# Performance work log

Measured on AMD Instinct MI355X. Metric: run time of the kernel, lower is better.

## Reference

```python
import jax, jax.numpy as jnp
import numpy as np
import math

B, NI, NU, D, H, MAXNB, T = 1024, 50000, 20000, 256, 4, 20, 1000


def _cosine_sqrt_ab():
    t = jnp.linspace(0.0, T, T + 1) / T
    ab = jnp.cos((t + 0.008) / 1.008 * math.pi / 2) ** 2
    ab = ab / ab[0]
    ab = ab[1:]
    return jnp.sqrt(ab), jnp.sqrt(1.0 - ab)


def _ln(x, g, b, eps=1e-5):
    m = jnp.mean(x, -1, keepdims=True)
    v = jnp.var(x, -1, keepdims=True)
    return (x - m) / jnp.sqrt(v + eps) * g + b


def _mha(q, k, v, wqkv, bqkv, wo, bo):
    # torch nn.MultiheadAttention (batch_first) with packed in_proj
    d = q.shape[-1]
    dh = d // H
    wq, wk, wv = jnp.split(wqkv, 3, axis=0)
    bq, bk, bv = jnp.split(bqkv, 3, axis=0)
    def heads(x, w, bb):
        y = x @ w.T + bb
        return y.reshape(x.shape[0], x.shape[1], H, dh).transpose(0, 2, 1, 3)
    qh, kh, vh = heads(q, wq, bq), heads(k, wk, bk), heads(v, wv, bv)
    att = jax.nn.softmax(jnp.einsum('bhqd,bhkd->bhqk', qh, kh) / math.sqrt(dh), axis=-1)
    o = jnp.einsum('bhqk,bhkd->bhqd', att, vh)
    o = o.transpose(0, 2, 1, 3).reshape(q.shape[0], q.shape[1], d)
    return o @ wo.T + bo


def setup_inputs() -> dict:
    key = jax.random.key(0)
    ks = iter(jax.random.split(key, 64))
    p = lambda shape, s=0.02: jax.random.normal(next(ks), shape, jnp.float32) * s
    inp = {}
    inp['x0'] = (jax.random.uniform(next(ks), (B, NI)) < 0.05).astype(jnp.float32)
    inp['user_ids'] = jax.random.randint(next(ks), (B,), 0, NU)
    inp['t'] = jax.random.randint(next(ks), (B,), 0, T)
    inp['noise'] = jax.random.normal(next(ks), (B, D), jnp.float32)
    inp['neighbor_idx'] = jax.random.randint(next(ks), (NU, MAXNB), 0, NI)
    inp['item_emb'] = p((NI, D), 0.01)
    inp['enc_w1'] = p((2 * D, NI), 0.01); inp['enc_b1'] = jnp.zeros((2 * D,))
    inp['enc_w2'] = p((D, 2 * D)); inp['enc_b2'] = jnp.zeros((D,))
    inp['dec_w1'] = p((2 * D, D)); inp['dec_b1'] = jnp.zeros((2 * D,))
    inp['dec_w2'] = p((NI, 2 * D)); inp['dec_b2'] = jnp.zeros((NI,))
    inp['up_w'] = p((D, D)); inp['up_b'] = jnp.zeros((D,))
    inp['ip_w'] = p((D, D)); inp['ip_b'] = jnp.zeros((D,))
    inp['te_w1'] = p((32, 1)); inp['te_b1'] = jnp.zeros((32,))
    inp['te_w2'] = p((D, 32)); inp['te_b2'] = jnp.zeros((D,))
    inp['ca_wqkv'] = p((3 * D, D)); inp['ca_bqkv'] = jnp.zeros((3 * D,))
    inp['ca_wo'] = p((D, D)); inp['ca_bo'] = jnp.zeros((D,))
    inp['sa_wqkv'] = p((3 * D, D)); inp['sa_bqkv'] = jnp.zeros((3 * D,))
    inp['sa_wo'] = p((D, D)); inp['sa_bo'] = jnp.zeros((D,))
    inp['n1_g'] = jnp.ones((D,)); inp['n1_b'] = jnp.zeros((D,))
    inp['n2_g'] = jnp.ones((D,)); inp['n2_b'] = jnp.zeros((D,))
    inp['ff_w1'] = p((2 * D, D)); inp['ff_b1'] = jnp.zeros((2 * D,))
    inp['ff_w2'] = p((D, 2 * D)); inp['ff_b2'] = jnp.zeros((D,))
    return inp


def reference(x0, user_ids, t, noise, neighbor_idx, item_emb,
              enc_w1, enc_b1, enc_w2, enc_b2, dec_w1, dec_b1, dec_w2, dec_b2,
              up_w, up_b, ip_w, ip_b, te_w1, te_b1, te_w2, te_b2,
              ca_wqkv, ca_bqkv, ca_wo, ca_bo, sa_wqkv, sa_bqkv, sa_wo, sa_bo,
              n1_g, n1_b, n2_g, n2_b, ff_w1, ff_b1, ff_w2, ff_b2):
    gelu = lambda x: jax.nn.gelu(x, approximate=False)
    # encoder: (B, NI) -> (B, D)
    z0 = gelu(x0 @ enc_w1.T + enc_b1) @ enc_w2.T + enc_b2
    sqrt_ab, sqrt_1ab = _cosine_sqrt_ab()
    z_t = sqrt_ab[t][:, None] * z0 + sqrt_1ab[t][:, None] * noise
    # vectorized padded neighbor gather: (B, MAXNB, D)
    nb = item_emb[neighbor_idx[user_ids]]
    t_norm = t.astype(jnp.float32) / T
    # denoiser
    q = (z_t @ up_w.T + up_b)[:, None, :]
    kv = nb @ ip_w.T + ip_b
    te = jax.nn.silu(t_norm[:, None] @ te_w1.T + te_b1) @ te_w2.T + te_b2
    q = q + te[:, None, :]
    ca = _mha(q, kv, kv, ca_wqkv, ca_bqkv, ca_wo, ca_bo)
    h = _ln(q + ca, n1_g, n1_b)[:, 0, :]
    sa = _mha(h[:, None], h[:, None], h[:, None], sa_wqkv, sa_bqkv, sa_wo, sa_bo)[:, 0, :]
    h = _ln(h + sa, n2_g, n2_b)
    z_pred = h + (gelu(h @ ff_w1.T + ff_b1) @ ff_w2.T + ff_b2)
    diff_loss = jnp.mean((z_pred - z0) ** 2)
    logits = gelu(z0 @ dec_w1.T + dec_b1) @ dec_w2.T + dec_b2
    recon = jnp.mean(jax.nn.softplus(logits) - logits * x0)
    return diff_loss + 0.1 * recon
```

## Files before the change

### kernel.cpp

```cpp
#include <hip/hip_runtime.h>
#include <math.h>

#define NI   50000
#define Tt   1000
#define KP   50176
#define MW   1568

typedef __bf16 bf16x8 __attribute__((ext_vector_type(8)));
typedef float  f32x4  __attribute__((ext_vector_type(4)));

__device__ __forceinline__ unsigned short f2bf(float f) {
  unsigned u = __float_as_uint(f);
  u += 0x7FFFu + ((u >> 16) & 1u);
  return (unsigned short)(u >> 16);
}
__device__ __forceinline__ float bf2f(unsigned short u) {
  return __uint_as_float(((unsigned)u) << 16);
}
__device__ __forceinline__ unsigned pack2(float a, float b) {
  return (unsigned)f2bf(a) | ((unsigned)f2bf(b) << 16);
}
__device__ __forceinline__ f32x4 mfma16(const unsigned short* a, const unsigned short* b, f32x4 c) {
  typedef unsigned short u16x8 __attribute__((ext_vector_type(8)));
  u16x8 av = *(const u16x8*)a;
  u16x8 bv = *(const u16x8*)b;
  return __builtin_amdgcn_mfma_f32_16x16x32_bf16(
      __builtin_bit_cast(bf16x8, av), __builtin_bit_cast(bf16x8, bv), c, 0, 0, 0);
}
__device__ __forceinline__ float gelu_f(float x) {
  return 0.5f * x * (1.f + erff(x * 0.70710678118654752f));
}

#define GLD16(gsrc, ldst) __builtin_amdgcn_global_load_lds( \
    (const __attribute__((address_space(1))) unsigned int*)(const void*)(gsrc), \
    (__attribute__((address_space(3))) unsigned int*)(void*)(ldst), 16, 0, 0)
#define GLD4(gsrc, ldst) __builtin_amdgcn_global_load_lds( \
    (const __attribute__((address_space(1))) unsigned int*)(const void*)(gsrc), \
    (__attribute__((address_space(3))) unsigned int*)(void*)(ldst), 4, 0, 0)

#define PIPE_FENCE() __builtin_amdgcn_sched_barrier(0)
#define RAW_BAR()    __builtin_amdgcn_s_barrier()

#define PC_BM 6272
#define PC_W1 19072

__global__ __launch_bounds__(256) void prep_crit(
    const float* __restrict__ x0, unsigned int* __restrict__ xmask,
    unsigned int* __restrict__ xmaskT,
    const float* __restrict__ enc_w1, unsigned short* __restrict__ w1b)
{
  __shared__ unsigned int T[32][8];
  const int id = blockIdx.x, tid = threadIdx.x;
  if (id < PC_BM) {
    const int rg = id / 196, wc = id % 196;
    const int r0 = rg * 32, w0 = wc * 8;
    const int rr = tid >> 3, wd = tid & 7;
    const int row = r0 + rr;
    const int gw = w0 + wd;
    const int cb = gw * 32;
    const float* rp = x0 + (size_t)row * NI + cb;
    unsigned wv = 0;
    if (cb + 32 <= NI) {
#pragma unroll
      for (int k = 0; k < 8; ++k) {
        float4 v = *(const float4*)(rp + k * 4);
        wv |= (v.x != 0.f ? 1u : 0u) << (k * 4) |
              (v.y != 0.f ? 2u : 0u) << (k * 4) |
              (v.z != 0.f ? 4u : 0u) << (k * 4) |
              (v.w != 0.f ? 8u : 0u) << (k * 4);
      }
    } else {
      for (int k = 0; k < 32; ++k)
        if (cb + k < NI && rp[k] != 0.f) wv |= 1u << k;
    }
    T[rr][wd] = wv;
    xmask[(size_t)row * MW + gw] = wv;
    __syncthreads();
    int wq = tid >> 5, r2 = tid & 31;
    xmaskT[(size_t)(w0 + wq) * 1024 + r0 + r2] = T[r2][wq];
  } else {
    int q = id - PC_BM;
    int r = q / 25, ch = q % 25;
    int c = ch * 2048 + tid * 8;
    if (c >= KP) return;
    const float* s = enc_w1 + (size_t)r * NI;
    uint4 o;
    if (c + 8 <= NI) {
      float4 a = *(const float4*)(s + c), b = *(const float4*)(s + c + 4);
      o.x = pack2(a.x, a.y); o.y = pack2(a.z, a.w);
      o.z = pack2(b.x, b.y); o.w = pack2(b.z, b.w);
    } else {
      float v[8];
#pragma unroll
      for (int i = 0; i < 8; ++i) v[i] = (c + i < NI) ? s[c + i] : 0.f;
      o.x = pack2(v[0], v[1]); o.y = pack2(v[2], v[3]);
      o.z = pack2(v[4], v[5]); o.w = pack2(v[6], v[7]);
    }
    *(uint4*)(w1b + (size_t)r * KP + c) = o;
  }
}

#define EF_ENC  1024
#define EF_W2N  2592
#define EF_MANY 3040
#define EF_COMP 3808
#define EF_TE   4832

__global__ __launch_bounds__(256) void enc_fused(
    const unsigned int* __restrict__ xmaskT,
    const unsigned short* __restrict__ Bw,
    float* __restrict__ P0, float* __restrict__ P1,
    const float* __restrict__ dec_w2, unsigned short* __restrict__ w2n,
    const float* s0a, const float* s1a, const float* s2a, const float* s3a,
    const float* s4a, const float* s5a, const float* s6a,
    unsigned short* d0a, unsigned short* d1a, unsigned short* d2a, unsigned short* d3a,
    unsigned short* d4a, unsigned short* d5a, unsigned short* d6a,
    const float* __restrict__ ca_wqkv, const float* __restrict__ ca_bqkv,
    const float* __restrict__ ip_w, const float* __restrict__ ip_b,
    const float* __restrict__ sa_wqkv, const float* __restrict__ sa_bqkv,
    const float* __restrict__ sa_wo, const float* __restrict__ sa_bo,
    unsigned short* __restrict__ Wkv, float* __restrict__ bkv,
    unsigned short* __restrict__ Wsa, float* __restrict__ bsa,
    const int* __restrict__ t,
    const float* __restrict__ te_w1, const float* __restrict__ te_b1,
    const float* __restrict__ te_w2, const float* __restrict__ te_b2,
    float* __restrict__ te, float* __restrict__ sab, float* __restrict__ s1ab)
{
  __shared__ __align__(16) unsigned short BsE[2][2][128 * 32];
  __shared__ __align__(16) unsigned short lut[256][8];
  __shared__ unsigned int mskb[2][2][128];
  __shared__ float sj[32];
  const int id = blockIdx.x, tid = threadIdx.x;

  if (id < EF_ENC) {
    const int g = (id & 7) + 8 * (id >> 6);
    const int m0 = ((id >> 3) & 7) * 128;
    const int n0 = (g & 3) * 128;
    const int kc = g >> 2;
    const int kb = kc * 1568;
    const int kw0 = kc * 49;
    const int w = tid >> 6, l = tid & 63;
    const int wm = (w >> 1) * 64, wn = (w & 1) * 64;
    const int fr = l & 15, fo = (l >> 4) * 8;
    const int s0 = tid, s1 = tid + 256;
    const unsigned short* Br0 = Bw + (size_t)(n0 + (s0 >> 2)) * KP + kb + (s0 & 3) * 8;
    const unsigned short* Br1 = Bw + (size_t)(n0 + (s1 >> 2)) * KP + kb + (s1 & 3) * 8;
    f32x4 acc[4][4] = {};

    {
      unsigned b = (unsigned)tid;
      uint4 q;
      q.x = (b & 1u   ? 0x3F80u : 0u) | (b & 2u   ? 0x3F800000u : 0u);
      q.y = (b & 4u   ? 0x3F80u : 0u) | (b & 8u   ? 0x3F800000u : 0u);
      q.z = (b & 16u  ? 0x3F80u : 0u) | (b & 32u  ? 0x3F800000u : 0u);
      q.w = (b & 64u  ? 0x3F80u : 0u) | (b & 128u ? 0x3F800000u : 0u);
      *(uint4*)&lut[tid][0] = q;
    }

#define STGF(IT, BUF) do {                                                  \
    GLD4(xmaskT + (size_t)(kw0 + (IT) * 2 + (w & 1)) * 1024                 \
                + m0 + (w >> 1) * 64 + l,                                   \
         &mskb[BUF][w & 1][(w >> 1) * 64]);                                 \
    GLD16(Br0 + (IT) * 64,      &BsE[BUF][0][s0 * 8]);                      \
    GLD16(Br1 + (IT) * 64,      &BsE[BUF][0][s1 * 8]);                      \
    GLD16(Br0 + (IT) * 64 + 32, &BsE[BUF][1][s0 * 8]);                      \
    GLD16(Br1 + (IT) * 64 + 32, &BsE[BUF][1][s1 * 8]); } while (0)

#define STGT(BUF) do {                                                      \
    GLD4(xmaskT + (size_t)(kw0 + 48) * 1024 + m0 + (w & 1) * 64 + l,        \
         &mskb[BUF][0][(w & 1) * 64]);                                      \
    GLD16(Br0 + 24 * 64, &BsE[BUF][0][s0 * 8]);                             \
    GLD16(Br1 + 24 * 64, &BsE[BUF][0][s1 * 8]); } while (0)

#define CMPH(BUF, KK) do {                                                  \
    const unsigned short *ap_[4], *bp_[4];                                  \
    _Pragma("unroll") for (int i_ = 0; i_ < 4; ++i_)                        \
      ap_[i_] = &lut[(mskb[BUF][KK][wm + 16 * i_ + fr] >> fo) & 0xFF][0];   \
    _Pragma("unroll") for (int j_ = 0; j_ < 4; ++j_)                        \
      bp_[j_] = &BsE[BUF][KK][(wn + 16 * j_ + fr) * 32 + fo];               \
    _Pragma("unroll") for (int i_ = 0; i_ < 4; ++i_)                        \
    _Pragma("unroll") for (int j_ = 0; j_ < 4; ++j_)                        \
      acc[i_][j_] = mfma16(ap_[i_], bp_[j_], acc[i_][j_]); } while (0)

    STGF(0, 0);
    STGF(1, 1);
    asm volatile("s_waitcnt vmcnt(5) lgkmcnt(0)" ::: "memory");
    PIPE_FENCE(); RAW_BAR(); PIPE_FENCE();
    for (int it = 0; it < 24; ++it) {
      CMPH(it & 1, 0);
      CMPH(it & 1, 1);
      PIPE_FENCE(); RAW_BAR(); PIPE_FENCE();
      if (it < 22) {
        STGF(it + 2, it & 1);
        asm volatile("s_waitcnt vmcnt(5)" ::: "memory");
      } else if (it == 22) {
        STGT(0);
        asm volatile("s_waitcnt vmcnt(3)" ::: "memory");
      } else {
        asm volatile("s_waitcnt vmcnt(0)" ::: "memory");
      }
      PIPE_FENCE(); RAW_BAR(); PIPE_FENCE();
    }
    CMPH(0, 0);
#undef STGF
#undef STGT
#undef CMPH

    const int cr = (l >> 4) * 4, cc = l & 15;
    float* Cp = ((kc < 16) ? P0 : P1) + (size_t)(kc & 15) * 524288;
#pragma unroll
    for (int i = 0; i < 4; ++i)
#pragma unroll
      for (int j = 0; j < 4; ++j) {
        int n = n0 + wn + 16 * j + cc;
#pragma unroll
        for (int r = 0; r < 4; ++r) {
          int m = m0 + wm + 16 * i + cr + r;
          Cp[(size_t)m * 512 + n] = acc[i][j][r];
        }
      }
  } else if (id < EF_W2N) {
    size_t b2 = id - EF_ENC;
    for (size_t e = (b2 * 256 + tid) * 8; e < 25600000u; e += (size_t)1568 * 256 * 8) {
      float4 a = *(const float4*)(dec_w2 + e), b = *(const float4*)(dec_w2 + e + 4);
      uint4 o;
      o.x = pack2(a.x, a.y); o.y = pack2(a.z, a.w);
      o.z = pack2(b.x, b.y); o.w = pack2(b.z, b.w);
      *(uint4*)(w2n + e) = o;
    }
  } else if (id < EF_MANY) {
    const float* srcs[7] = {s0a, s1a, s2a, s3a, s4a, s5a, s6a};
    unsigned short* dsts[7] = {d0a, d1a, d2a, d3a, d4a, d5a, d6a};
    const int ns[7] = {131072, 65536, 65536, 65536, 131072, 131072, 131072};
    int q = id - EF_W2N;
    int j = q >> 6;
    int i = ((q & 63) * 256 + tid) * 8;
    if (i >= ns[j]) return;
    float4 a = *(const float4*)(srcs[j] + i), b = *(const float4*)(srcs[j] + i + 4);
    uint4 o;
    o.x = pack2(a.x, a.y); o.y = pack2(a.z, a.w);
    o.z = pack2(b.x, b.y); o.w = pack2(b.z, b.w);
    *(uint4*)(dsts[j] + i) = o;
  } else if (id < EF_COMP) {
    int b = id - EF_MANY, k = tid;
    if (b < 512) {
      const float* wrow = ca_wqkv + (size_t)(256 + b) * 256;
      float s = 0.f;
      for (int c = 0; c < 256; ++c) s += wrow[c] * ip_w[c * 256 + k];
      Wkv[b * 256 + k] = f2bf(s);
      if (k == 0) {
        float sb = 0.f;
        for (int c = 0; c < 256; ++c) sb += wrow[c] * ip_b[c];
        bkv[b] = sb + ca_bqkv[256 + b];
      }
    } else {
      int i = b - 512;
      const float* worow = sa_wo + (size_t)i * 256;
      float s = 0.f;
      for (int c = 0; c < 256; ++c) s += worow[c] * sa_wqkv[(512 + c) * 256 + k];
      Wsa[i * 256 + k] = f2bf(s);
      if (k == 0) {
        float sb = 0.f;
        for (int c = 0; c < 256; ++c) sb += worow[c] * sa_bqkv[512 + c];
        bsa[i] = sb + sa_bo[i];
      }
    }
  } else {
    int b = id - EF_COMP, d = tid;
    int ti = t[b];
    float tn = (float)ti / (float)Tt;
    if (d < 32) {
      float a = tn * te_w1[d] + te_b1[d];
      sj[d] = a / (1.f + __expf(-a));
    }
    if (d == 0) {
      double tt = (double)(ti + 1) / (double)Tt;
      double c  = cos((tt + 0.008) / 1.008 * M_PI * 0.5);
      double c0 = cos((0.008) / 1.008 * M_PI * 0.5);
      double ab = (c * c) / (c0 * c0);
      sab[b]  = (float)sqrt(ab);
      s1ab[b] = (float)sqrt(1.0 - ab);
    }
    __syncthreads();
    float accv = te_b2[d];
#pragma unroll
    for (int j = 0; j < 32; ++j) accv += sj[j] * te_w2[d * 32 + j];
    te[(size_t)b * 256 + d] = accv;
  }
}

__global__ __launch_bounds__(256) void gemm128(
    const unsigned short* __restrict__ A, int lda,
    const unsigned short* __restrict__ Bw, int ldb,
    const float* __restrict__ bias, void* __restrict__ Cv, int ldc, int K)
{
  __shared__ __align__(16) unsigned short As[128 * 32];
  __shared__ __align__(16) unsigned short Bs[128 * 32];
  const int tid = threadIdx.x;
  const int m0 = blockIdx.x * 128, n0 = blockIdx.y * 128;
  const int iters = K >> 5;
  const int w = tid >> 6, l = tid & 63;
  const int wm = (w >> 1) * 64, wn = (w & 1) * 64;
  const int fr = l & 15, fo = (l >> 4) * 8;
  const int s0 = tid, s1 = tid + 256;
  f32x4 acc[4][4] = {};
  for (int it = 0; it < iters; ++it) {
    int k0 = it * 32;
    __syncthreads();
    GLD16(A  + (size_t)(m0 + (s0 >> 2)) * lda + k0 + (s0 & 3) * 8, &As[s0 * 8]);
    GLD16(A  + (size_t)(m0 + (s1 >> 2)) * lda + k0 + (s1 & 3) * 8, &As[s1 * 8]);
    GLD16(Bw + (size_t)(n0 + (s0 >> 2)) * ldb + k0 + (s0 & 3) * 8, &Bs[s0 * 8]);
    GLD16(Bw + (size_t)(n0 + (s1 >> 2)) * ldb + k0 + (s1 & 3) * 8, &Bs[s1 * 8]);
    __syncthreads();
    const unsigned short *ap[4], *bp[4];
#pragma unroll
    for (int i = 0; i < 4; ++i) {
      ap[i] = &As[(wm + 16 * i + fr) * 32 + fo];
      bp[i] = &Bs[(wn + 16 * i + fr) * 32 + fo];
    }
#pragma unroll
    for (int i = 0; i < 4; ++i)
#pragma unroll
      for (int j = 0; j < 4; ++j)
        acc[i][j] = mfma16(ap[i], bp[j], acc[i][j]);
  }
  const int cr = (l >> 4) * 4, cc = l & 15;
  unsigned short* Cb = (unsigned short*)Cv;
#pragma unroll
  for (int j = 0; j < 4; ++j) {
    int n = n0 + wn + 16 * j + cc;
    float bv = bias[n];
#pragma unroll
    for (int i = 0; i < 4; ++i)
#pragma unroll
      for (int r = 0; r < 4; ++r) {
        int m = m0 + wm + 16 * i + cr + r;
        Cb[(size_t)m * ldc + n] = f2bf(acc[i][j][r] + bv);
      }
  }
}

__global__ __launch_bounds__(256) void dec_gemm(
    const unsigned short* __restrict__ A,
    const unsigned short* __restrict__ Bw,
    const float* __restrict__ bias,
    const unsigned int* __restrict__ xmask, float* __restrict__ loss, int Nvalid)
{
  __shared__ __align__(16) unsigned short As[128 * 32];
  __shared__ __align__(16) unsigned short Bs[256 * 32];
  __shared__ unsigned int msk[128][8];
  __shared__ float red[4];
  const int tid = threadIdx.x;
  const int id = blockIdx.x;
  const int n = (id & 7) + 8 * (id >> 6);
  if (n >= 196) return;
  const int m0 = ((id >> 3) & 7) * 128;
  const int n0 = n * 256;
  const int w = tid >> 6, l = tid & 63;
  const int wm = (w >> 1) * 64, wn = (w & 1) * 128;
  const int fr = l & 15, fo = (l >> 4) * 8;
  const int s0 = tid, s1 = tid + 256;
  const int b0 = tid, b1 = tid + 256, b2 = tid + 512, b3 = tid + 768;
  f32x4 acc[4][8] = {};
  for (int it = 0; it < 16; ++it) {
    int k0 = it * 32;
    __syncthreads();
    GLD16(A  + (size_t)(m0 + (s0 >> 2)) * 512 + k0 + (s0 & 3) * 8, &As[s0 * 8]);
    GLD16(A  + (size_t)(m0 + (s1 >> 2)) * 512 + k0 + (s1 & 3) * 8, &As[s1 * 8]);
    GLD16(Bw + (size_t)(n0 + (b0 >> 2)) * 512 + k0 + (b0 & 3) * 8, &Bs[b0 * 8]);
    GLD16(Bw + (size_t)(n0 + (b1 >> 2)) * 512 + k0 + (b1 & 3) * 8, &Bs[b1 * 8]);
    GLD16(Bw + (size_t)(n0 + (b2 >> 2)) * 512 + k0 + (b2 & 3) * 8, &Bs[b2 * 8]);
    GLD16(Bw + (size_t)(n0 + (b3 >> 2)) * 512 + k0 + (b3 & 3) * 8, &Bs[b3 * 8]);
    __syncthreads();
    const unsigned short *ap[4], *bp[8];
#pragma unroll
    for (int i = 0; i < 4; ++i)
      ap[i] = &As[(wm + 16 * i + fr) * 32 + fo];
#pragma unroll
    for (int j = 0; j < 8; ++j)
      bp[j] = &Bs[(wn + 16 * j + fr) * 32 + fo];
#pragma unroll
    for (int i = 0; i < 4; ++i)
#pragma unroll
      for (int j = 0; j < 8; ++j)
        acc[i][j] = mfma16(ap[i], bp[j], acc[i][j]);
  }
  {
    int row = tid >> 1, p = tid & 1;
    *(uint4*)&msk[row][p * 4] =
        *(const uint4*)(xmask + (size_t)(m0 + row) * MW + (n0 >> 5) + p * 4);
  }
  __syncthreads();
  const int cr = (l >> 4) * 4, cc = l & 15;
  float ts = 0.f;
#pragma unroll
  for (int j = 0; j < 8; ++j) {
    int nl = wn + 16 * j + cc;
    int nn = n0 + nl;
    if (nn < Nvalid) {
      float bv = bias[nn];
#pragma unroll
      for (int i = 0; i < 4; ++i)
#pragma unroll
        for (int r = 0; r < 4; ++r) {
          int ml = wm + 16 * i + cr + r;
          float lg = acc[i][j][r] + bv;
          float sp = fmaxf(lg, 0.f) + __logf(1.f + __expf(-fabsf(lg)));
          unsigned word = msk[ml][nl >> 5];
          ts += sp - (((word >> (nl & 31)) & 1u) ? lg : 0.f);
        }
    }
  }
  for (int off = 32; off > 0; off >>= 1) ts += __shfl_xor(ts, off);
  if (l == 0) red[w] = ts;
  __syncthreads();
  if (tid == 0) atomicAdd(loss, red[0] + red[1] + red[2] + red[3]);
}

template<int EPI>
__global__ __launch_bounds__(256) void gemm64(
    const unsigned short* __restrict__ A, int lda,
    const unsigned short* __restrict__ Bw, int ldb,
    const float* __restrict__ bias, void* __restrict__ Cv, int ldc, int K,
    const void* __restrict__ R0, const void* __restrict__ R1, const void* __restrict__ R2,
    void* __restrict__ W0, void* __restrict__ W1, float* __restrict__ loss)
{
  __shared__ __align__(16) unsigned short As[64 * 32];
  __shared__ __align__(16) unsigned short Bs[64 * 32];
  __shared__ float red[4];
  const int tid = threadIdx.x;
  const int m0 = blockIdx.x * 64, n0 = blockIdx.y * 64;
  const int w = tid >> 6, l = tid & 63;
  const int wm = (w >> 1) * 32, wn = (w & 1) * 32;
  const int fr = l & 15, fo = (l >> 4) * 8;
  const int srow = tid >> 2, scol = (tid & 3) * 8;
  f32x4 acc[2][2] = {};
  for (int k0 = 0; k0 < K; k0 += 32) {
    __syncthreads();
    GLD16(A  + (size_t)(m0 + srow) * lda + k0 + scol, &As[tid * 8]);
    GLD16(Bw + (size_t)(n0 + srow) * ldb + k0 + scol, &Bs[tid * 8]);
    __syncthreads();
    const unsigned short* ap0 = &As[(wm +      fr) * 32 + fo];
    const unsigned short* ap1 = &As[(wm + 16 + fr) * 32 + fo];
    const unsigned short* bp0 = &Bs[(wn +      fr) * 32 + fo];
    const unsigned short* bp1 = &Bs[(wn + 16 + fr) * 32 + fo];
    acc[0][0] = mfma16(ap0, bp0, acc[0][0]);
    acc[0][1] = mfma16(ap0, bp1, acc[0][1]);
    acc[1][0] = mfma16(ap1, bp0, acc[1][0]);
    acc[1][1] = mfma16(ap1, bp1, acc[1][1]);
  }
  const int cr = (l >> 4) * 4, cc = l & 15;
  float ts = 0.f;
#pragma unroll
  for (int i = 0; i < 2; ++i)
#pragma unroll
    for (int j = 0; j < 2; ++j) {
      int n = n0 + wn + 16 * j + cc;
      float bv = bias[n];
#pragma unroll
      for (int r = 0; r < 4; ++r) {
        int m = m0 + wm + 16 * i + cr + r;
        float v = acc[i][j][r] + bv;
        size_t idx = (size_t)m * ldc + n;
        if (EPI == 0) ((float*)Cv)[idx] = v;
        if (EPI == 1) ((unsigned short*)Cv)[idx] = f2bf(v);
        if (EPI == 2) ((unsigned short*)Cv)[idx] = f2bf(gelu_f(v));
        if (EPI == 3) {
          ((float*)Cv)[idx] = v;
          ((unsigned short*)W0)[idx] = f2bf(v);
          float zt = ((const float*)R1)[m] * v +
                     ((const float*)R2)[m] * ((const float*)R0)[idx];
          ((unsigned short*)W1)[idx] = f2bf(zt);
        }
        if (EPI == 4) {
          v += ((const float*)R0)[idx];
          ((unsigned short*)Cv)[idx] = f2bf(v);
        }
        if (EPI == 5) {
          v += bf2f(((const unsigned short*)R0)[idx]);
          float d = v - ((const float*)R1)[idx];
          ts += d * d;
        }
      }
    }
  if (EPI == 5) {
    for (int off = 32; off > 0; off >>= 1) ts += __shfl_xor(ts, off);
    if (l == 0) red[w] = ts;
    __syncthreads();
    if (tid == 0) atomicAdd(loss, red[0] + red[1] + red[2] + red[3]);
  }
}

__global__ __launch_bounds__(256) void h1_epi(const float* __restrict__ P0,
                                              const float* __restrict__ P1,
                                              const float* __restrict__ b,
                                              unsigned short* __restrict__ H) {
  int i = blockIdx.x * 256 + threadIdx.x;
  float s = b[i & 511];
#pragma unroll
  for (int k = 0; k < 16; ++k) s += P0[(size_t)k * 524288 + i];
#pragma unroll
  for (int k = 0; k < 16; ++k) s += P1[(size_t)k * 524288 + i];
  H[i] = f2bf(gelu_f(s));
}

__global__ __launch_bounds__(256) void gather_nb(
    const int* __restrict__ uid, const int* __restrict__ nidx,
    const float* __restrict__ emb, unsigned short* __restrict__ nb)
{
  int b = blockIdx.x, d = threadIdx.x;
  const int* np = nidx + uid[b] * 20;
#pragma unroll
  for (int j = 0; j < 20; ++j) {
    int idx = np[j];
    nb[((size_t)b * 20 + j) * 256 + d] = f2bf(emb[(size_t)idx * 256 + d]);
  }
}

__global__ __launch_bounds__(256) void attn_k(
    const float* __restrict__ qh, const unsigned short* __restrict__ kvh,
    unsigned short* __restrict__ o)
{
  int b = blockIdx.x, tid = threadIdx.x;
  int h = tid >> 6, d = tid & 63;
  float qv = qh[(size_t)b * 256 + h * 64 + d];
  const unsigned short* kbase = kvh + (size_t)b * 20 * 512 + h * 64 + d;
  const unsigned short* vbase = kbase + 256;
  float s[20];
#pragma unroll
  for (int k = 0; k < 20; ++k) {
    float p = qv * bf2f(kbase[k * 512]);
    for (int off = 32; off > 0; off >>= 1) p += __shfl_xor(p, off);
    s[k] = p * 0.125f;
  }
  float mx = s[0];
#pragma unroll
  for (int k = 1; k < 20; ++k) mx = fmaxf(mx, s[k]);
  float sum = 0.f;
#pragma unroll
  for (int k = 0; k < 20; ++k) { s[k] = __expf(s[k] - mx); sum += s[k]; }
  float inv = 1.f / sum;
  float ov = 0.f;
#pragma unroll
  for (int k = 0; k < 20; ++k) ov += s[k] * bf2f(vbase[k * 512]);
  o[(size_t)b * 256 + h * 64 + d] = f2bf(ov * inv);
}

__global__ __launch_bounds__(256) void ln_k(
    const unsigned short* __restrict__ X, const unsigned short* __restrict__ Y,
    const float* __restrict__ g, const float* __restrict__ bb,
    unsigned short* __restrict__ out)
{
  __shared__ float rs[4], rs2[4];
  int b = blockIdx.x, d = threadIdx.x;
  size_t i = (size_t)b * 256 + d;
  float v = bf2f(X[i]) + bf2f(Y[i]);
  float s = v, s2 = v * v;
  for (int off = 32; off > 0; off >>= 1) { s += __shfl_xor(s, off); s2 += __shfl_xor(s2, off); }
  int w = d >> 6, l = d & 63;
  if (l == 0) { rs[w] = s; rs2[w] = s2; }
  __syncthreads();
  s  = rs[0] + rs[1] + rs[2] + rs[3];
  s2 = rs2[0] + rs2[1] + rs2[2] + rs2[3];
  float mean = s * (1.f / 256.f);
  float var  = s2 * (1.f / 256.f) - mean * mean;
  out[i] = f2bf((v - mean) * rsqrtf(var + 1e-5f) * g[d] + bb[d]);
}

__global__ void final_k(const float* __restrict__ scal, float* __restrict__ out) {
  out[0] = scal[0] * (1.f / (1024.f * 256.f)) + 0.1f * scal[1] * (1.f / (1024.f * 50000.f));
}

extern "C" void kernel_launch(void* const* d_in, const int* in_sizes, int n_in,
                              void* d_out, int out_size, void* d_ws, size_t ws_size,
                              hipStream_t stream) {
  const float* x0      = (const float*)d_in[0];
  const int*   uid     = (const int*)  d_in[1];
  const int*   t       = (const int*)  d_in[2];
  const float* noise   = (const float*)d_in[3];
  const int*   nidx    = (const int*)  d_in[4];
  const float* item_emb= (const float*)d_in[5];
  const float* enc_w1  = (const float*)d_in[6];
  const float* enc_b1  = (const float*)d_in[7];
  const float* enc_w2  = (const float*)d_in[8];
  const float* enc_b2  = (const float*)d_in[9];
  const float* dec_w1  = (const float*)d_in[10];
  const float* dec_b1  = (const float*)d_in[11];
  const float* dec_w2  = (const float*)d_in[12];
  const float* dec_b2  = (const float*)d_in[13];
  const float* up_w    = (const float*)d_in[14];
  const float* up_b    = (const float*)d_in[15];
  const float* ip_w    = (const float*)d_in[16];
  const float* ip_b    = (const float*)d_in[17];
  const float* te_w1   = (const float*)d_in[18];
  const float* te_b1   = (const float*)d_in[19];
  const float* te_w2   = (const float*)d_in[20];
  const float* te_b2   = (const float*)d_in[21];
  const float* ca_wqkv = (const float*)d_in[22];
  const float* ca_bqkv = (const float*)d_in[23];
  const float* ca_wo   = (const float*)d_in[24];
  const float* ca_bo   = (const float*)d_in[25];
  const float* sa_wqkv = (const float*)d_in[26];
  const float* sa_bqkv = (const float*)d_in[27];
  const float* sa_wo   = (const float*)d_in[28];
  const float* sa_bo   = (const float*)d_in[29];
  const float* n1_g    = (const float*)d_in[30];
  const float* n1_b    = (const float*)d_in[31];
  const float* n2_g    = (const float*)d_in[32];
  const float* n2_b    = (const float*)d_in[33];
  const float* ff_w1   = (const float*)d_in[34];
  const float* ff_b1   = (const float*)d_in[35];
  const float* ff_w2   = (const float*)d_in[36];
  const float* ff_b2   = (const float*)d_in[37];
  (void)in_sizes; (void)n_in; (void)out_size; (void)ws_size;

  float* ws   = (float*)d_ws;
  float* scal = ws;
  float* sab  = ws + 4;
  float* s1ab = sab + 1024;
  float* te   = s1ab + 1024;
  float* qhf  = te + 262144;
  float* z0f  = qhf + 262144;
  float* bkv  = z0f + 262144;
  float* bsa  = bkv + 512;
  unsigned int* xmask = (unsigned int*)(bsa + 256);
  unsigned short* sh  = (unsigned short*)(xmask + 1024 * MW);
  float*          OUTp = (float*)sh;
  unsigned short* nbb  = sh;
  unsigned short* kvhb = nbb + 5242880;
  unsigned short* f1b  = kvhb + 10485760;
  unsigned short* Gb   = f1b + 524288;
  unsigned short* x0b  = Gb + 524288;
  unsigned short* w2n  = x0b;
  unsigned int*   xmaskT = (unsigned int*)(x0b + 26214400);
  unsigned short* w1b  = x0b + (size_t)1024 * KP;
  unsigned short* H1b  = w1b + (size_t)512 * KP;
  unsigned short* z0b  = H1b + 524288;
  unsigned short* ztb  = z0b + 262144;
  unsigned short* qpb  = ztb + 262144;
  unsigned short* ob   = qpb + 262144;
  unsigned short* cab  = ob  + 262144;
  unsigned short* hb   = cab + 262144;
  unsigned short* saob = hb  + 262144;
  unsigned short* h2b  = saob+ 262144;
  unsigned short* enc_w2b = h2b + 262144;
  unsigned short* up_wb   = enc_w2b + 131072;
  unsigned short* ca_wqb  = up_wb + 65536;
  unsigned short* ca_wob  = ca_wqb + 65536;
  unsigned short* ff_w1b  = ca_wob + 65536;
  unsigned short* ff_w2b  = ff_w1b + 131072;
  unsigned short* dec_w1b = ff_w2b + 131072;
  unsigned short* Wkv     = dec_w1b + 131072;
  unsigned short* Wsab    = Wkv + 131072;
  float*          OUTp2   = (float*)(Wsab + 131072);

  hipMemsetAsync(scal, 0, 4 * sizeof(float), stream);

  prep_crit<<<PC_W1, 256, 0, stream>>>(x0, xmask, xmaskT, enc_w1, w1b);

  enc_fused<<<EF_TE, 256, 0, stream>>>(
      xmaskT, w1b, OUTp, OUTp2,
      dec_w2, w2n,
      enc_w2, up_w, ca_wqkv, ca_wo, ff_w1, ff_w2, dec_w1,
      enc_w2b, up_wb, ca_wqb, ca_wob, ff_w1b, ff_w2b, dec_w1b,
      ca_wqkv, ca_bqkv, ip_w, ip_b, sa_wqkv, sa_bqkv, sa_wo, sa_bo,
      Wkv, bkv, Wsab, bsa,
      t, te_w1, te_b1, te_w2, te_b2, te, sab, s1ab);
  h1_epi<<<2048, 256, 0, stream>>>(OUTp, OUTp2, enc_b1, H1b);

  gather_nb<<<1024, 256, 0, stream>>>(uid, nidx, item_emb, nbb);
  gemm128<<<dim3(160, 4), 256, 0, stream>>>(
      nbb, 256, Wkv, 256, bkv, kvhb, 512, 256);

  gemm64<3><<<dim3(16, 4), 256, 0, stream>>>(
      H1b, 512, enc_w2b, 512, enc_b2, z0f, 256, 512, noise, sab, s1ab, z0b, ztb, nullptr);

  gemm64<4><<<dim3(16, 4), 256, 0, stream>>>(
      ztb, 256, up_wb, 256, up_b, qpb, 256, 256, te, nullptr, nullptr, nullptr, nullptr, nullptr);
  gemm64<0><<<dim3(16, 4), 256, 0, stream>>>(
      qpb, 256, ca_wqb, 256, ca_bqkv, qhf, 256, 256,
      nullptr, nullptr, nullptr, nullptr, nullptr, nullptr);

  attn_k<<<1024, 256, 0, stream>>>(qhf, kvhb, ob);
  gemm64<1><<<dim3(16, 4), 256, 0, stream>>>(
      ob, 256, ca_wob, 256, ca_bo, cab, 256, 256,
      nullptr, nullptr, nullptr, nullptr, nullptr, nullptr);
  ln_k<<<1024, 256, 0, stream>>>(qpb, cab, n1_g, n1_b, hb);

  gemm64<1><<<dim3(16, 4), 256, 0, stream>>>(
      hb, 256, Wsab, 256, bsa, saob, 256, 256,
      nullptr, nullptr, nullptr, nullptr, nullptr, nullptr);
  ln_k<<<1024, 256, 0, stream>>>(hb, saob, n2_g, n2_b, h2b);

  gemm64<2><<<dim3(16, 8), 256, 0, stream>>>(
      h2b, 256, ff_w1b, 256, ff_b1, f1b, 512, 256,
      nullptr, nullptr, nullptr, nullptr, nullptr, nullptr);
  gemm64<5><<<dim3(16, 4), 256, 0, stream>>>(
      f1b, 512, ff_w2b, 512, ff_b2, nullptr, 256, 512,
      h2b, z0f, nullptr, nullptr, nullptr, &scal[0]);

  gemm64<2><<<dim3(16, 8), 256, 0, stream>>>(
      z0b, 256, dec_w1b, 256, dec_b1, Gb, 512, 256,
      nullptr, nullptr, nullptr, nullptr, nullptr, nullptr);
  dec_gemm<<<1600, 256, 0, stream>>>(
      Gb, w2n, dec_b2, xmask, &scal[1], NI);

  final_k<<<1, 1, 0, stream>>>(scal, (float*)d_out);
}
```

Baseline: 894.0 us.

## Shrink decoder GEMM N-tile to 128 and load 64-wide K chunks per barrier

The fused decoder GEMM with softplus-loss epilogue now uses 128x128 tiles instead of 128x256, which doubles the grid to 3136 blocks and halves the accumulator registers per thread. Each iteration also loads two 32-wide K slices into separate shared buffers, so there are half as many barrier pairs. Smaller tiles should raise occupancy and balance load across CUs, at the cost of more A-operand reloads and a smaller mask load per block.

Result: faster. 794.3 us (-11.2%).

```diff
diff --git a/kernel.cpp b/kernel.cpp
--- a/kernel.cpp
+++ b/kernel.cpp
@@ -346,55 +346,62 @@
     const float* __restrict__ bias,
     const unsigned int* __restrict__ xmask, float* __restrict__ loss, int Nvalid)
 {
-  __shared__ __align__(16) unsigned short As[128 * 32];
-  __shared__ __align__(16) unsigned short Bs[256 * 32];
-  __shared__ unsigned int msk[128][8];
+  __shared__ __align__(16) unsigned short As[2][128 * 32];
+  __shared__ __align__(16) unsigned short Bs[2][128 * 32];
+  __shared__ unsigned int msk[128][4];
   __shared__ float red[4];
   const int tid = threadIdx.x;
   const int id = blockIdx.x;
   const int n = (id & 7) + 8 * (id >> 6);
-  if (n >= 196) return;
+  if (n >= 391) return;
   const int m0 = ((id >> 3) & 7) * 128;
-  const int n0 = n * 256;
+  const int n0 = n * 128;
   const int w = tid >> 6, l = tid & 63;
-  const int wm = (w >> 1) * 64, wn = (w & 1) * 128;
+  const int wm = (w >> 1) * 64, wn = (w & 1) * 64;
   const int fr = l & 15, fo = (l >> 4) * 8;
   const int s0 = tid, s1 = tid + 256;
-  const int b0 = tid, b1 = tid + 256, b2 = tid + 512, b3 = tid + 768;
-  f32x4 acc[4][8] = {};
-  for (int it = 0; it < 16; ++it) {
-    int k0 = it * 32;
-    __syncthreads();
-    GLD16(A  + (size_t)(m0 + (s0 >> 2)) * 512 + k0 + (s0 & 3) * 8, &As[s0 * 8]);
-    GLD16(A  + (size_t)(m0 + (s1 >> 2)) * 512 + k0 + (s1 & 3) * 8, &As[s1 * 8]);
-    GLD16(Bw + (size_t)(n0 + (b0 >> 2)) * 512 + k0 + (b0 & 3) * 8, &Bs[b0 * 8]);
-    GLD16(Bw + (size_t)(n0 + (b1 >> 2)) * 512 + k0 + (b1 & 3) * 8, &Bs[b1 * 8]);
-    GLD16(Bw + (size_t)(n0 + (b2 >> 2)) * 512 + k0 + (b2 & 3) * 8, &Bs[b2 * 8]);
-    GLD16(Bw + (size_t)(n0 + (b3 >> 2)) * 512 + k0 + (b3 & 3) * 8, &Bs[b3 * 8]);
-    __syncthreads();
-    const unsigned short *ap[4], *bp[8];
-#pragma unroll
-    for (int i = 0; i < 4; ++i)
-      ap[i] = &As[(wm + 16 * i + fr) * 32 + fo];
-#pragma unroll
-    for (int j = 0; j < 8; ++j)
-      bp[j] = &Bs[(wn + 16 * j + fr) * 32 + fo];
-#pragma unroll
-    for (int i = 0; i < 4; ++i)
-#pragma unroll
-      for (int j = 0; j < 8; ++j)
-        acc[i][j] = mfma16(ap[i], bp[j], acc[i][j]);
+  const unsigned short* Ar0 = A  + (size_t)(m0 + (s0 >> 2)) * 512 + (s0 & 3) * 8;
+  const unsigned short* Ar1 = A  + (size_t)(m0 + (s1 >> 2)) * 512 + (s1 & 3) * 8;
+  const unsigned short* Br0 = Bw + (size_t)(n0 + (s0 >> 2)) * 512 + (s0 & 3) * 8;
+  const unsigned short* Br1 = Bw + (size_t)(n0 + (s1 >> 2)) * 512 + (s1 & 3) * 8;
+  f32x4 acc[4][4] = {};
+  for (int it = 0; it < 8; ++it) {
+    int k0 = it * 64;
+    __syncthreads();
+    GLD16(Ar0 + k0,      &As[0][s0 * 8]);
+    GLD16(Ar1 + k0,      &As[0][s1 * 8]);
+    GLD16(Br0 + k0,      &Bs[0][s0 * 8]);
+    GLD16(Br1 + k0,      &Bs[0][s1 * 8]);
+    GLD16(Ar0 + k0 + 32, &As[1][s0 * 8]);
+    GLD16(Ar1 + k0 + 32, &As[1][s1 * 8]);
+    GLD16(Br0 + k0 + 32, &Bs[1][s0 * 8]);
+    GLD16(Br1 + k0 + 32, &Bs[1][s1 * 8]);
+    __syncthreads();
+#pragma unroll
+    for (int h = 0; h < 2; ++h) {
+      const unsigned short *ap[4], *bp[4];
+#pragma unroll
+      for (int i = 0; i < 4; ++i) {
+        ap[i] = &As[h][(wm + 16 * i + fr) * 32 + fo];
+        bp[i] = &Bs[h][(wn + 16 * i + fr) * 32 + fo];
+      }
+#pragma unroll
+      for (int i = 0; i < 4; ++i)
+#pragma unroll
+        for (int j = 0; j < 4; ++j)
+          acc[i][j] = mfma16(ap[i], bp[j], acc[i][j]);
+    }
   }
   {
     int row = tid >> 1, p = tid & 1;
-    *(uint4*)&msk[row][p * 4] =
-        *(const uint4*)(xmask + (size_t)(m0 + row) * MW + (n0 >> 5) + p * 4);
+    *(uint2*)&msk[row][p * 2] =
+        *(const uint2*)(xmask + (size_t)(m0 + row) * MW + (n0 >> 5) + p * 2);
   }
   __syncthreads();
   const int cr = (l >> 4) * 4, cc = l & 15;
   float ts = 0.f;
 #pragma unroll
-  for (int j = 0; j < 8; ++j) {
+  for (int j = 0; j < 4; ++j) {
     int nl = wn + 16 * j + cc;
     int nn = n0 + nl;
     if (nn < Nvalid) {
@@ -702,7 +709,7 @@
   gemm64<2><<<dim3(16, 8), 256, 0, stream>>>(
       z0b, 256, dec_w1b, 256, dec_b1, Gb, 512, 256,
       nullptr, nullptr, nullptr, nullptr, nullptr, nullptr);
-  dec_gemm<<<1600, 256, 0, stream>>>(
+  dec_gemm<<<3136, 256, 0, stream>>>(
       Gb, w2n, dec_b2, xmask, &scal[1], NI);
 
   final_k<<<1, 1, 0, stream>>>(scal, (float*)d_out);
```
